# Kernel tuning notes

Measured on AMD Instinct MI355X. Metric: run time of the kernel, lower is better.

The kernel has to match this reference:

```python
import jax, jax.numpy as jnp
import numpy as np

B, C, N, IC = 4, 64, 4096, 32  # batch, in_channels(=g_channels), nodes, inter_channels


def setup_inputs() -> dict:
    key = jax.random.key(0)
    ks = jax.random.split(key, 8)
    s_c = (2.0 / C) ** 0.5   # kaiming-ish scales
    s_i = (2.0 / C) ** 0.5
    x = jax.random.normal(ks[0], (B, C, N), dtype=jnp.float32)
    g_w = jax.random.normal(ks[1], (C, C), dtype=jnp.float32) * s_c      # g: 1x1 conv (out=C, in=C)
    g_b = jnp.zeros((C,), dtype=jnp.float32)
    theta_w = jax.random.normal(ks[2], (IC, C), dtype=jnp.float32) * s_i  # theta: (out=IC, in=C)
    theta_b = jnp.zeros((IC,), dtype=jnp.float32)
    phi_w = jax.random.normal(ks[3], (IC, C), dtype=jnp.float32) * s_i
    phi_b = jnp.zeros((IC,), dtype=jnp.float32)
    cp_w = jax.random.normal(ks[4], (2 * IC,), dtype=jnp.float32) * (2.0 / (2 * IC)) ** 0.5  # concat_project 1x1 conv, no bias
    C_k = jnp.zeros((N, N), dtype=jnp.float32)  # learned adjacency bias, init zeros
    return {"x": x, "g_w": g_w, "g_b": g_b, "theta_w": theta_w, "theta_b": theta_b,
            "phi_w": phi_w, "phi_b": phi_b, "cp_w": cp_w, "C_k": C_k}


def reference(x, g_w, g_b, theta_w, theta_b, phi_w, phi_b, cp_w, C_k):
    # 1x1 convs are plain GEMMs over the node dim
    g_x = jnp.einsum('oc,bcn->bno', g_w, x) + g_b            # (B, N, C)
    th = jnp.einsum('oc,bcn->bon', theta_w, x) + theta_b[:, None]  # (B, IC, N)
    ph = jnp.einsum('oc,bcn->bon', phi_w, x) + phi_b[:, None]      # (B, IC, N)
    # concat_project on [theta_i ; phi_j] with a 1x1 conv is algebraically an outer sum:
    # f[b,i,j] = w_th . theta[b,:,i] + w_ph . phi[b,:,j]
    a = jnp.einsum('c,bcn->bn', cp_w[:IC], th)  # (B, N)
    p = jnp.einsum('c,bcn->bn', cp_w[IC:], ph)  # (B, N)
    f = a[:, :, None] + p[:, None, :]           # (B, N, N)
    attention = jax.nn.softmax(jax.nn.leaky_relu(f, negative_slope=0.2), axis=-1) + C_k
    y = jnp.einsum('bij,bjo->boi', attention, g_x)  # (B, C, N)
    return y
```

## Files before the change

kernel.cpp:

```cpp
#include <hip/hip_runtime.h>


#define B  4
#define C  64
#define N  4096
#define IC 32
#define NS 4104
#define NR 4097
#define MAGIC 0x13572468

#define OFF_FLAG   248
#define OFF_A      256
#define OFF_P      (OFF_A + B*N)
#define OFF_Q      (OFF_P + B*N)
#define OFF_PERM   (OFF_Q + B*N)
#define OFF_PRES   (OFF_PERM + B*N)
#define OFF_SUFS   (OFF_PRES + B*NS)
#define OFF_S1     (OFF_SUFS + B*NS)
#define OFF_S2     (OFF_S1 + B*64*64)
#define OFF_GX     (OFF_S2 + B*64*64)
#define OFF_PREG   (OFF_GX + B*N*64)
#define OFF_SUFG   (OFF_PREG + B*NR*64)

__global__ __launch_bounds__(256) void k1_gx(
    const float* __restrict__ x, const float* __restrict__ g_w,
    const float* __restrict__ g_b, const float* __restrict__ theta_w,
    const float* __restrict__ theta_b, const float* __restrict__ phi_w,
    const float* __restrict__ phi_b, const float* __restrict__ cp_w,
    const float* __restrict__ Ck, float* __restrict__ ws) {
  __shared__ float gwT[C * C];
  __shared__ float xl[C * 16];
  __shared__ float lu[C], lv[C], cst[2];
  const int tid = threadIdx.x;
  const int b = blockIdx.x >> 8;
  const int n0 = (blockIdx.x & 255) << 4;
  for (int idx = tid; idx < C * C; idx += 256) {
    int o = idx >> 6, cc = idx & 63;
    gwT[cc * C + o] = g_w[idx];
  }
  for (int idx = tid; idx < C * 16; idx += 256) {
    int cc = idx >> 4, nn = idx & 15;
    xl[idx] = x[(size_t)((b << 6) + cc) * N + n0 + nn];
  }
  if (tid < 64) {
    float u = 0.f;
    for (int k = 0; k < IC; ++k) u += cp_w[k] * theta_w[k * C + tid];
    lu[tid] = u;
  } else if (tid < 128) {
    int c = tid - 64;
    float v = 0.f;
    for (int k = 0; k < IC; ++k) v += cp_w[IC + k] * phi_w[k * C + c];
    lv[c] = v;
  } else if (tid == 128) {
    float ca = 0.f, cp2 = 0.f;
    for (int k = 0; k < IC; ++k) { ca += cp_w[k] * theta_b[k]; cp2 += cp_w[IC + k] * phi_b[k]; }
    cst[0] = ca; cst[1] = cp2;
  }
  __syncthreads();
  if (tid < 16) {
    float au = cst[0], pu = cst[1];
    for (int cc = 0; cc < C; ++cc) {
      float xv = xl[cc * 16 + tid];
      au += lu[cc] * xv;
      pu += lv[cc] * xv;
    }
    ws[OFF_A + (b << 12) + n0 + tid] = au;
    ws[OFF_P + (b << 12) + n0 + tid] = pu;
  }
  const int o = tid & 63, g4 = tid >> 6;
  float bb = g_b[o];
  float acc0 = bb, acc1 = bb, acc2 = bb, acc3 = bb;
  for (int cc = 0; cc < C; ++cc) {
    float gv = gwT[cc * C + o];
    const float* xr = &xl[cc * 16 + (g4 << 2)];
    acc0 += gv * xr[0]; acc1 += gv * xr[1]; acc2 += gv * xr[2]; acc3 += gv * xr[3];
  }
  float* gx = ws + OFF_GX + (size_t)((b << 12) + n0 + (g4 << 2)) * C + o;
  gx[0] = acc0; gx[64] = acc1; gx[128] = acc2; gx[192] = acc3;
  const float4* c4 = (const float4*)Ck;
  bool nz = false;
  int idx = (blockIdx.x << 8) + tid;
  for (int t = 0; t < 16; ++t) {
    float4 v = c4[idx];
    nz |= (v.x != 0.f) | (v.y != 0.f) | (v.z != 0.f) | (v.w != 0.f);
    idx += 262144;
  }
  if (__any(nz) && (tid & 63) == 0)
    atomicExch((int*)ws + OFF_FLAG, MAGIC);
}

__global__ __launch_bounds__(1024) void k2_rank(float* __restrict__ ws) {
  __shared__ float lp[N];
  __shared__ int partials[32][33];
  const int tid = threadIdx.x;
  const int b = blockIdx.x >> 7;
  const int rg = blockIdx.x & 127;
  const float* p = ws + OFF_P + b * N;
  ((float4*)lp)[tid] = ((const float4*)p)[tid];
  const int row = tid & 31, chunk = tid >> 5;
  const int i = (rg << 5) + row;
  __syncthreads();
  const float my = lp[i];
  const int c0 = chunk << 7;
  const float4* lp4 = (const float4*)(lp + c0);
  int r0 = 0, r1 = 0, r2 = 0, r3 = 0;
  for (int j = 0; j < 32; ++j) {
    float4 v = lp4[j];
    int k = c0 + (j << 2);
    r0 += (v.x < my) || (v.x == my && (k + 0) < i);
    r1 += (v.y < my) || (v.y == my && (k + 1) < i);
    r2 += (v.z < my) || (v.z == my && (k + 2) < i);
    r3 += (v.w < my) || (v.w == my && (k + 3) < i);
  }
  partials[row][chunk] = (r0 + r1) + (r2 + r3);
  __syncthreads();
  if (tid < 32) {
    int rank = 0;
#pragma unroll
    for (int c = 0; c < 32; ++c) rank += partials[tid][c];
    const int ii = (rg << 5) + tid;
    ws[OFF_Q + (b << 12) + rank] = lp[ii];
    ((int*)ws)[OFF_PERM + (b << 12) + rank] = ii;
  }
}

__global__ __launch_bounds__(1024) void k3_scan_chunks(float* __restrict__ ws) {
  __shared__ float sA[1024], sB[1024];
  const int tid = threadIdx.x;
  const int bid = blockIdx.x;
  if (bid < B) {
    const int b = bid;
    float* wt2 = sA;
    float* wt1 = sA + 16;
    float* wo2 = sA + 32;
    float* wo1 = sA + 49;
    const float* q = ws + OFF_Q + b * N;
    const float4 qv4 = ((const float4*)q)[tid];
    float e1r[4], e2r[4];
    e2r[0] = expf(0.2f * qv4.x); e1r[0] = expf(qv4.x);
    e2r[1] = expf(0.2f * qv4.y); e1r[1] = expf(qv4.y);
    e2r[2] = expf(0.2f * qv4.z); e1r[2] = expf(qv4.z);
    e2r[3] = expf(0.2f * qv4.w); e1r[3] = expf(qv4.w);
    float s2 = e2r[0] + e2r[1] + e2r[2] + e2r[3];
    float s1 = e1r[0] + e1r[1] + e1r[2] + e1r[3];
    const int lane = tid & 63, wave = tid >> 6;
    float x2 = s2, x1 = s1;
    for (int off = 1; off < 64; off <<= 1) {
      float t2 = __shfl_up(x2, off, 64);
      float t1 = __shfl_up(x1, off, 64);
      if (lane >= off) { x2 += t2; x1 += t1; }
    }
    if (lane == 63) { wt2[wave] = x2; wt1[wave] = x1; }
    __syncthreads();
    if (wave == 0 && lane < 17) {
      float a2 = 0.f, a1 = 0.f;
      for (int w = 0; w < 16; ++w) {
        if (w < lane) { a2 += wt2[w]; a1 += wt1[w]; }
      }
      wo2[lane] = a2; wo1[lane] = a1;
    }
    __syncthreads();
    const float excl2 = wo2[wave] + (x2 - s2);
    const float incl1 = wo1[wave] + x1;
    const float tot1 = wo1[16];
    float* PreS = ws + OFF_PRES + b * NS;
    float* SufS = ws + OFF_SUFS + b * NS;
    const int base = tid << 2;
    float run = excl2;
#pragma unroll
    for (int j = 0; j < 4; ++j) { PreS[base + j] = run; run += e2r[j]; }
    if (tid == 1023) PreS[N] = run;
    run = tot1 - incl1;
#pragma unroll
    for (int j = 3; j >= 0; --j) { run += e1r[j]; SufS[base + j] = run; }
    if (tid == 1023) SufS[N] = 0.f;
  } else {
    const int b2 = bid - B;
    const int b = b2 >> 6, c = b2 & 63;
    const int o = tid & 63, kk = tid >> 6;
    const float* q = ws + OFF_Q + b * N;
    const int* perm = (const int*)ws + OFF_PERM + b * N;
    const float* gx = ws + OFF_GX + ((size_t)b << 18);
    float p1 = 0.f, p2 = 0.f;
    const int k0 = (c << 6) + (kk << 2);
    for (int r = 0; r < 4; ++r) {
      int k = k0 + r;
      float qv = q[k];
      float g = gx[((size_t)perm[k] << 6) + o];
      p1 += expf(qv) * g;
      p2 += expf(0.2f * qv) * g;
    }
    sA[(kk << 6) + o] = p2;
    sB[(kk << 6) + o] = p1;
    __syncthreads();
    if (tid < 64) {
      float t2 = 0.f, t1 = 0.f;
#pragma unroll
      for (int g = 0; g < 16; ++g) { t2 += sA[(g << 6) + o]; t1 += sB[(g << 6) + o]; }
      ws[OFF_S2 + (size_t)(((b << 6) + c) << 6) + o] = t2;
      ws[OFF_S1 + (size_t)(((b << 6) + c) << 6) + o] = t1;
    }
  }
}

__global__ __launch_bounds__(1024) void k4_prefix(float* __restrict__ ws) {
  __shared__ float sA[1024], sB[1024];
  const int tid = threadIdx.x;
  const int b = blockIdx.x >> 6, c = blockIdx.x & 63;
  const int o = tid & 63, kk = tid >> 6;
  float offp = 0.f, offs = 0.f;
  {
    const float* S1 = ws + OFF_S1 + ((size_t)b << 12);
    const float* S2 = ws + OFF_S2 + ((size_t)b << 12);
    for (int cc = 0; cc < 64; ++cc) {
      float v2 = S2[(cc << 6) + o];
      float v1 = S1[(cc << 6) + o];
      offp += (cc < c) ? v2 : 0.f;
      offs += (cc > c) ? v1 : 0.f;
    }
  }
  const float* q = ws + OFF_Q + b * N;
  const int* perm = (const int*)ws + OFF_PERM + b * N;
  const float* gx = ws + OFF_GX + ((size_t)b << 18);
  float* PreG = ws + OFF_PREG + (size_t)b * NR * 64;
  float* SufG = ws + OFF_SUFG + (size_t)b * NR * 64;
  const int k0 = (c << 6) + (kk << 2);
  float w1[4], w2[4];
  float p1 = 0.f, p2 = 0.f;
  for (int r = 0; r < 4; ++r) {
    float qq = q[k0 + r];
    float gg = gx[((size_t)perm[k0 + r] << 6) + o];
    w1[r] = expf(qq) * gg;
    w2[r] = expf(0.2f * qq) * gg;
    p1 += w1[r]; p2 += w2[r];
  }
  sA[(kk << 6) + o] = p2;
  sB[(kk << 6) + o] = p1;
  __syncthreads();
  for (int kp = 0; kp < kk; ++kp) offp += sA[(kp << 6) + o];
  for (int kp = kk + 1; kp < 16; ++kp) offs += sB[(kp << 6) + o];
  float run = offp;
#pragma unroll
  for (int r = 0; r < 4; ++r) { PreG[(size_t)(k0 + r) * 64 + o] = run; run += w2[r]; }
  if (c == 63 && kk == 15) PreG[(size_t)N * 64 + o] = run;
  run = offs;
#pragma unroll
  for (int r = 3; r >= 0; --r) { run += w1[r]; SufG[(size_t)(k0 + r) * 64 + o] = run; }
  if (c == 0 && kk == 0) SufG[(size_t)N * 64 + o] = 0.f;
}

__global__ __launch_bounds__(1024) void k5_out(const float* __restrict__ Ck,
                                               float* __restrict__ ws,
                                               float* __restrict__ y) {
  __shared__ float lq[N];
  const int tid = threadIdx.x;
  const int b = blockIdx.x >> 6, rg = blockIdx.x & 63;
  const float4* qs = (const float4*)(ws + OFF_Q + b * N);
  ((float4*)lq)[tid] = qs[tid];
  __syncthreads();
  const int io = tid & 63, og = tid >> 6;
  const int i = (rg << 6) + io;
  float ai = ws[OFF_A + (b << 12) + i];
  float thr = -ai;
  int lo = 0, hi = N;
  while (lo < hi) { int m = (lo + hi) >> 1; if (lq[m] <= thr) lo = m + 1; else hi = m; }
  const int k = lo;
  float e1 = expf(ai), e2 = expf(0.2f * ai);
  float den = e1 * ws[OFF_SUFS + b * NS + k] + e2 * ws[OFF_PRES + b * NS + k];
  float inv = 1.0f / den;
  float4 pv = ((const float4*)(ws + OFF_PREG + ((size_t)b * NR + k) * 64))[og];
  float4 sv = ((const float4*)(ws + OFF_SUFG + ((size_t)b * NR + k) * 64))[og];
  float* yb = y + ((size_t)((b << 6) + (og << 2))) * N + i;
  yb[0]             = (e1 * sv.x + e2 * pv.x) * inv;
  yb[(size_t)N]     = (e1 * sv.y + e2 * pv.y) * inv;
  yb[(size_t)2 * N] = (e1 * sv.z + e2 * pv.z) * inv;
  yb[(size_t)3 * N] = (e1 * sv.w + e2 * pv.w) * inv;
  if (((const volatile int*)ws)[OFF_FLAG] == MAGIC) {
    __syncthreads();
    const int it = rg;
    const int o = tid & 63, jj = tid >> 6;
    const float* gx = ws + OFF_GX + ((size_t)b << 18);
    float (*red)[64] = (float(*)[64])lq;
    for (int ii = 0; ii < 64; ++ii) {
      int irow = (it << 6) + ii;
      float acc = 0.f;
      for (int j = jj; j < N; j += 16)
        acc += Ck[(size_t)irow * N + j] * gx[((size_t)j << 6) + o];
      red[jj][o] = acc;
      __syncthreads();
      if (jj == 0) {
        float s = 0.f;
#pragma unroll
        for (int g = 0; g < 16; ++g) s += red[g][o];
        y[((size_t)((b << 6) + o)) * N + irow] += s;
      }
      __syncthreads();
    }
  }
}

extern "C" void kernel_launch(void* const* d_in, const int* in_sizes, int n_in,
                              void* d_out, int out_size, void* d_ws, size_t ws_size,
                              hipStream_t stream) {
  (void)in_sizes; (void)n_in; (void)out_size; (void)ws_size;
  const float* x       = (const float*)d_in[0];
  const float* g_w     = (const float*)d_in[1];
  const float* g_b     = (const float*)d_in[2];
  const float* theta_w = (const float*)d_in[3];
  const float* theta_b = (const float*)d_in[4];
  const float* phi_w   = (const float*)d_in[5];
  const float* phi_b   = (const float*)d_in[6];
  const float* cp_w    = (const float*)d_in[7];
  const float* Ck      = (const float*)d_in[8];
  float* ws = (float*)d_ws;
  float* y  = (float*)d_out;

  hipLaunchKernelGGL(k1_gx, dim3(1024), dim3(256), 0, stream,
                     x, g_w, g_b, theta_w, theta_b, phi_w, phi_b, cp_w, Ck, ws);
  hipLaunchKernelGGL(k2_rank, dim3(512), dim3(1024), 0, stream, ws);
  hipLaunchKernelGGL(k3_scan_chunks, dim3(B + B * 64), dim3(1024), 0, stream, ws);
  hipLaunchKernelGGL(k4_prefix, dim3(B * 64), dim3(1024), 0, stream, ws);
  hipLaunchKernelGGL(k5_out, dim3(B * 64), dim3(1024), 0, stream, Ck, ws, y);
}
```

Measured before the change: 150.5 us.

## Fuse chunk scan and prefix kernels into one with redundant per-block chunk sums

Merges the scan/chunk-sum kernel and the prefix kernel into a single launch of 128 blocks. Each block recomputes the exp tables into LDS, every chunk sum for its batch, and the scalar prefix/suffix sums, then writes PreG/SufG for two chunks. This removes one kernel launch and the global round trip through S1/S2. In exchange each block redundantly gathers the whole batch's gx rows, about 1 MB per block, and the grid shrinks to 128 blocks.

```diff
diff --git a/kernel.cpp b/kernel.cpp
--- a/kernel.cpp
+++ b/kernel.cpp
@@ -124,129 +124,124 @@
   }
 }
 
-__global__ __launch_bounds__(1024) void k3_scan_chunks(float* __restrict__ ws) {
-  __shared__ float sA[1024], sB[1024];
+__global__ __launch_bounds__(1024) void k34_prefix(float* __restrict__ ws) {
+  __shared__ float smem[16384];
+  float* le1 = smem;
+  float* le2 = smem + 4096;
+  float* S1L = smem + 8192;
+  float* S2L = smem + 12288;
+  float* cs1  = S1L;
+  float* cs2  = S1L + 64;
+  float* cum1 = S1L + 128;
+  float* cum2 = S1L + 192;
+  float* tots = S1L + 256;
   const int tid = threadIdx.x;
-  const int bid = blockIdx.x;
-  if (bid < B) {
-    const int b = bid;
-    float* wt2 = sA;
-    float* wt1 = sA + 16;
-    float* wo2 = sA + 32;
-    float* wo1 = sA + 49;
-    const float* q = ws + OFF_Q + b * N;
-    const float4 qv4 = ((const float4*)q)[tid];
-    float e1r[4], e2r[4];
-    e2r[0] = expf(0.2f * qv4.x); e1r[0] = expf(qv4.x);
-    e2r[1] = expf(0.2f * qv4.y); e1r[1] = expf(qv4.y);
-    e2r[2] = expf(0.2f * qv4.z); e1r[2] = expf(qv4.z);
-    e2r[3] = expf(0.2f * qv4.w); e1r[3] = expf(qv4.w);
-    float s2 = e2r[0] + e2r[1] + e2r[2] + e2r[3];
-    float s1 = e1r[0] + e1r[1] + e1r[2] + e1r[3];
-    const int lane = tid & 63, wave = tid >> 6;
-    float x2 = s2, x1 = s1;
+  const int b = blockIdx.x >> 5, cg = blockIdx.x & 31;
+  const float* q = ws + OFF_Q + (b << 12);
+  const float4 q4 = ((const float4*)q)[tid];
+  const float e1r0 = expf(q4.x), e1r1 = expf(q4.y), e1r2 = expf(q4.z), e1r3 = expf(q4.w);
+  const float e2r0 = expf(0.2f * q4.x), e2r1 = expf(0.2f * q4.y),
+              e2r2 = expf(0.2f * q4.z), e2r3 = expf(0.2f * q4.w);
+  const int k4 = tid << 2;
+  float4 t1v = {e1r0, e1r1, e1r2, e1r3};
+  float4 t2v = {e2r0, e2r1, e2r2, e2r3};
+  *(float4*)&le1[k4] = t1v;
+  *(float4*)&le2[k4] = t2v;
+  float s1 = (e1r0 + e1r1) + (e1r2 + e1r3);
+  float s2 = (e2r0 + e2r1) + (e2r2 + e2r3);
+  for (int off = 8; off; off >>= 1) {
+    s1 += __shfl_down(s1, off, 16);
+    s2 += __shfl_down(s2, off, 16);
+  }
+  if ((tid & 15) == 0) { cs1[tid >> 4] = s1; cs2[tid >> 4] = s2; }
+  __syncthreads();
+  if (tid < 64) {
+    float a1s = 0.f, a2s = 0.f;
+    for (int c2 = 0; c2 < 64; ++c2) {
+      float v1 = cs1[c2], v2 = cs2[c2];
+      a1s += (c2 < tid) ? v1 : 0.f;
+      a2s += (c2 < tid) ? v2 : 0.f;
+    }
+    cum1[tid] = a1s; cum2[tid] = a2s;
+    if (tid == 63) { tots[0] = a1s + cs1[63]; tots[1] = a2s + cs2[63]; }
+  }
+  __syncthreads();
+  if (tid < 128) {
+    const int k = (cg << 7) + tid, c = k >> 6, lane = tid & 63;
+    float x1 = le1[k], x2 = le2[k];
+    const float e1v = x1, e2v = x2;
     for (int off = 1; off < 64; off <<= 1) {
-      float t2 = __shfl_up(x2, off, 64);
-      float t1 = __shfl_up(x1, off, 64);
-      if (lane >= off) { x2 += t2; x1 += t1; }
-    }
-    if (lane == 63) { wt2[wave] = x2; wt1[wave] = x1; }
-    __syncthreads();
-    if (wave == 0 && lane < 17) {
-      float a2 = 0.f, a1 = 0.f;
-      for (int w = 0; w < 16; ++w) {
-        if (w < lane) { a2 += wt2[w]; a1 += wt1[w]; }
-      }
-      wo2[lane] = a2; wo1[lane] = a1;
-    }
-    __syncthreads();
-    const float excl2 = wo2[wave] + (x2 - s2);
-    const float incl1 = wo1[wave] + x1;
-    const float tot1 = wo1[16];
-    float* PreS = ws + OFF_PRES + b * NS;
-    float* SufS = ws + OFF_SUFS + b * NS;
-    const int base = tid << 2;
-    float run = excl2;
-#pragma unroll
-    for (int j = 0; j < 4; ++j) { PreS[base + j] = run; run += e2r[j]; }
-    if (tid == 1023) PreS[N] = run;
-    run = tot1 - incl1;
-#pragma unroll
-    for (int j = 3; j >= 0; --j) { run += e1r[j]; SufS[base + j] = run; }
-    if (tid == 1023) SufS[N] = 0.f;
-  } else {
-    const int b2 = bid - B;
-    const int b = b2 >> 6, c = b2 & 63;
-    const int o = tid & 63, kk = tid >> 6;
-    const float* q = ws + OFF_Q + b * N;
-    const int* perm = (const int*)ws + OFF_PERM + b * N;
-    const float* gx = ws + OFF_GX + ((size_t)b << 18);
+      float u1 = __shfl_up(x1, off, 64);
+      float u2 = __shfl_up(x2, off, 64);
+      if (lane >= off) { x1 += u1; x2 += u2; }
+    }
+    ws[OFF_PRES + b * NS + k] = cum2[c] + (x2 - e2v);
+    ws[OFF_SUFS + b * NS + k] = tots[0] - (cum1[c] + (x1 - e1v));
+    if (cg == 31 && tid == 127) ws[OFF_PRES + b * NS + N] = tots[1];
+    if (cg == 0 && tid == 0)    ws[OFF_SUFS + b * NS + N] = 0.f;
+  }
+  __syncthreads();
+  const int l16 = tid & 15, krow = tid >> 4;
+  const int* perm = (const int*)ws + OFF_PERM + (b << 12);
+  const float* gx = ws + OFF_GX + ((size_t)b << 18);
+  float4 a1 = {0.f, 0.f, 0.f, 0.f}, a2 = {0.f, 0.f, 0.f, 0.f};
+  const int kb = krow << 6;
+  const int jrot = (krow & 3) << 4;
+  for (int jj = 0; jj < 64; ++jj) {
+    const int k = kb + ((jj + jrot) & 63);
+    const float4 g = *(const float4*)(gx + ((size_t)perm[k] << 6) + (l16 << 2));
+    const float e1 = le1[k], e2 = le2[k];
+    a1.x += e1 * g.x; a1.y += e1 * g.y; a1.z += e1 * g.z; a1.w += e1 * g.w;
+    a2.x += e2 * g.x; a2.y += e2 * g.y; a2.z += e2 * g.z; a2.w += e2 * g.w;
+  }
+  *(float4*)&S1L[(krow << 6) + (l16 << 2)] = a1;
+  *(float4*)&S2L[(krow << 6) + (l16 << 2)] = a2;
+  __syncthreads();
+  const int o = tid & 63, kk = tid >> 6;
+  const int c0 = cg << 1;
+  float op0 = 0.f, os0 = 0.f, op1 = 0.f, os1 = 0.f;
+  for (int cc = 0; cc < 64; ++cc) {
+    const float v2 = S2L[(cc << 6) + o];
+    const float v1 = S1L[(cc << 6) + o];
+    op0 += (cc < c0) ? v2 : 0.f;       os0 += (cc > c0) ? v1 : 0.f;
+    op1 += (cc <= c0) ? v2 : 0.f;      os1 += (cc > c0 + 1) ? v1 : 0.f;
+  }
+  __syncthreads();
+  float* sA = S1L;
+  float* sB = S1L + 1024;
+  float* PreG = ws + OFF_PREG + (size_t)b * NR * 64;
+  float* SufG = ws + OFF_SUFG + (size_t)b * NR * 64;
+#pragma unroll
+  for (int ci = 0; ci < 2; ++ci) {
+    const int c = c0 + ci;
+    const int k0 = (c << 6) + (kk << 2);
+    float w1[4], w2[4];
     float p1 = 0.f, p2 = 0.f;
-    const int k0 = (c << 6) + (kk << 2);
+#pragma unroll
     for (int r = 0; r < 4; ++r) {
-      int k = k0 + r;
-      float qv = q[k];
-      float g = gx[((size_t)perm[k] << 6) + o];
-      p1 += expf(qv) * g;
-      p2 += expf(0.2f * qv) * g;
+      const int k = k0 + r;
+      const float g = gx[((size_t)perm[k] << 6) + o];
+      w1[r] = le1[k] * g;
+      w2[r] = le2[k] * g;
+      p1 += w1[r]; p2 += w2[r];
     }
     sA[(kk << 6) + o] = p2;
     sB[(kk << 6) + o] = p1;
     __syncthreads();
-    if (tid < 64) {
-      float t2 = 0.f, t1 = 0.f;
-#pragma unroll
-      for (int g = 0; g < 16; ++g) { t2 += sA[(g << 6) + o]; t1 += sB[(g << 6) + o]; }
-      ws[OFF_S2 + (size_t)(((b << 6) + c) << 6) + o] = t2;
-      ws[OFF_S1 + (size_t)(((b << 6) + c) << 6) + o] = t1;
-    }
-  }
-}
-
-__global__ __launch_bounds__(1024) void k4_prefix(float* __restrict__ ws) {
-  __shared__ float sA[1024], sB[1024];
-  const int tid = threadIdx.x;
-  const int b = blockIdx.x >> 6, c = blockIdx.x & 63;
-  const int o = tid & 63, kk = tid >> 6;
-  float offp = 0.f, offs = 0.f;
-  {
-    const float* S1 = ws + OFF_S1 + ((size_t)b << 12);
-    const float* S2 = ws + OFF_S2 + ((size_t)b << 12);
-    for (int cc = 0; cc < 64; ++cc) {
-      float v2 = S2[(cc << 6) + o];
-      float v1 = S1[(cc << 6) + o];
-      offp += (cc < c) ? v2 : 0.f;
-      offs += (cc > c) ? v1 : 0.f;
-    }
-  }
-  const float* q = ws + OFF_Q + b * N;
-  const int* perm = (const int*)ws + OFF_PERM + b * N;
-  const float* gx = ws + OFF_GX + ((size_t)b << 18);
-  float* PreG = ws + OFF_PREG + (size_t)b * NR * 64;
-  float* SufG = ws + OFF_SUFG + (size_t)b * NR * 64;
-  const int k0 = (c << 6) + (kk << 2);
-  float w1[4], w2[4];
-  float p1 = 0.f, p2 = 0.f;
-  for (int r = 0; r < 4; ++r) {
-    float qq = q[k0 + r];
-    float gg = gx[((size_t)perm[k0 + r] << 6) + o];
-    w1[r] = expf(qq) * gg;
-    w2[r] = expf(0.2f * qq) * gg;
-    p1 += w1[r]; p2 += w2[r];
-  }
-  sA[(kk << 6) + o] = p2;
-  sB[(kk << 6) + o] = p1;
-  __syncthreads();
-  for (int kp = 0; kp < kk; ++kp) offp += sA[(kp << 6) + o];
-  for (int kp = kk + 1; kp < 16; ++kp) offs += sB[(kp << 6) + o];
-  float run = offp;
-#pragma unroll
-  for (int r = 0; r < 4; ++r) { PreG[(size_t)(k0 + r) * 64 + o] = run; run += w2[r]; }
-  if (c == 63 && kk == 15) PreG[(size_t)N * 64 + o] = run;
-  run = offs;
-#pragma unroll
-  for (int r = 3; r >= 0; --r) { run += w1[r]; SufG[(size_t)(k0 + r) * 64 + o] = run; }
-  if (c == 0 && kk == 0) SufG[(size_t)N * 64 + o] = 0.f;
+    float op = ci ? op1 : op0;
+    float os = ci ? os1 : os0;
+    for (int kp = 0; kp < kk; ++kp) op += sA[(kp << 6) + o];
+    for (int kp = kk + 1; kp < 16; ++kp) os += sB[(kp << 6) + o];
+    float run = op;
+#pragma unroll
+    for (int r = 0; r < 4; ++r) { PreG[(size_t)(k0 + r) * 64 + o] = run; run += w2[r]; }
+    if (c == 63 && kk == 15) PreG[(size_t)N * 64 + o] = run;
+    run = os;
+#pragma unroll
+    for (int r = 3; r >= 0; --r) { run += w1[r]; SufG[(size_t)(k0 + r) * 64 + o] = run; }
+    if (c == 0 && kk == 0) SufG[(size_t)N * 64 + o] = 0.f;
+    __syncthreads();
+  }
 }
 
 __global__ __launch_bounds__(1024) void k5_out(const float* __restrict__ Ck,
@@ -318,7 +313,6 @@
   hipLaunchKernelGGL(k1_gx, dim3(1024), dim3(256), 0, stream,
                      x, g_w, g_b, theta_w, theta_b, phi_w, phi_b, cp_w, Ck, ws);
   hipLaunchKernelGGL(k2_rank, dim3(512), dim3(1024), 0, stream, ws);
-  hipLaunchKernelGGL(k3_scan_chunks, dim3(B + B * 64), dim3(1024), 0, stream, ws);
-  hipLaunchKernelGGL(k4_prefix, dim3(B * 64), dim3(1024), 0, stream, ws);
+  hipLaunchKernelGGL(k34_prefix, dim3(B * 32), dim3(1024), 0, stream, ws);
   hipLaunchKernelGGL(k5_out, dim3(B * 64), dim3(1024), 0, stream, Ck, ws, y);
 }
```

Result: slower. 161.8 us (+7.5%).

## Spread the C_k nonzero scan across the first four kernels

Applied to the files above, without the earlier changes.

The full scan of the 64MB C_k matrix for nonzero entries used to sit in k1 as 16 sequential float4 loads per thread. It is now split into quarters, with k1, k2, k3 and k4 each loading one quarter early and checking it at the end. The aim is to overlap this bandwidth-bound read with each kernel's own compute and to issue the loads up front. The cost is more live registers and extra loads in the 1024-thread kernels.

```diff
diff --git a/kernel.cpp b/kernel.cpp
--- a/kernel.cpp
+++ b/kernel.cpp
@@ -8,6 +8,7 @@
 #define NS 4104
 #define NR 4097
 #define MAGIC 0x13572468
+#define CKQ 1048576
 
 #define OFF_FLAG   248
 #define OFF_A      256
@@ -22,6 +23,8 @@
 #define OFF_PREG   (OFF_GX + B*N*64)
 #define OFF_SUFG   (OFF_PREG + B*NR*64)
 
+#define CK_NZ(v) ((v.x != 0.f) | (v.y != 0.f) | (v.z != 0.f) | (v.w != 0.f))
+
 __global__ __launch_bounds__(256) void k1_gx(
     const float* __restrict__ x, const float* __restrict__ g_w,
     const float* __restrict__ g_b, const float* __restrict__ theta_w,
@@ -34,6 +37,13 @@
   const int tid = threadIdx.x;
   const int b = blockIdx.x >> 8;
   const int n0 = (blockIdx.x & 255) << 4;
+  const float4* c4 = (const float4*)Ck;
+  float4 ck0, ck1, ck2, ck3;
+  {
+    int idx = (blockIdx.x << 8) + tid;
+    ck0 = c4[idx]; ck1 = c4[idx + 262144];
+    ck2 = c4[idx + 524288]; ck3 = c4[idx + 786432];
+  }
   for (int idx = tid; idx < C * C; idx += 256) {
     int o = idx >> 6, cc = idx & 63;
     gwT[cc * C + o] = g_w[idx];
@@ -77,24 +87,24 @@
   }
   float* gx = ws + OFF_GX + (size_t)((b << 12) + n0 + (g4 << 2)) * C + o;
   gx[0] = acc0; gx[64] = acc1; gx[128] = acc2; gx[192] = acc3;
-  const float4* c4 = (const float4*)Ck;
-  bool nz = false;
-  int idx = (blockIdx.x << 8) + tid;
-  for (int t = 0; t < 16; ++t) {
-    float4 v = c4[idx];
-    nz |= (v.x != 0.f) | (v.y != 0.f) | (v.z != 0.f) | (v.w != 0.f);
-    idx += 262144;
-  }
+  bool nz = CK_NZ(ck0) | CK_NZ(ck1) | CK_NZ(ck2) | CK_NZ(ck3);
   if (__any(nz) && (tid & 63) == 0)
     atomicExch((int*)ws + OFF_FLAG, MAGIC);
 }
 
-__global__ __launch_bounds__(1024) void k2_rank(float* __restrict__ ws) {
+__global__ __launch_bounds__(1024) void k2_rank(const float* __restrict__ Ck,
+                                                float* __restrict__ ws) {
   __shared__ float lp[N];
   __shared__ int partials[32][33];
   const int tid = threadIdx.x;
   const int b = blockIdx.x >> 7;
   const int rg = blockIdx.x & 127;
+  const float4* c4 = (const float4*)Ck + CKQ;
+  float4 ck0, ck1;
+  {
+    int idx = (blockIdx.x << 10) + tid;
+    ck0 = c4[idx]; ck1 = c4[idx + 524288];
+  }
   const float* p = ws + OFF_P + b * N;
   ((float4*)lp)[tid] = ((const float4*)p)[tid];
   const int row = tid & 31, chunk = tid >> 5;
@@ -122,12 +132,25 @@
     ws[OFF_Q + (b << 12) + rank] = lp[ii];
     ((int*)ws)[OFF_PERM + (b << 12) + rank] = ii;
   }
-}
-
-__global__ __launch_bounds__(1024) void k3_scan_chunks(float* __restrict__ ws) {
+  bool nz = CK_NZ(ck0) | CK_NZ(ck1);
+  if (__any(nz) && (tid & 63) == 0)
+    atomicExch((int*)ws + OFF_FLAG, MAGIC);
+}
+
+__global__ __launch_bounds__(1024) void k3_scan_chunks(const float* __restrict__ Ck,
+                                                       float* __restrict__ ws) {
   __shared__ float sA[1024], sB[1024];
   const int tid = threadIdx.x;
   const int bid = blockIdx.x;
+  const float4* c4 = (const float4*)Ck + 2 * CKQ;
+  float4 ck0 = {0.f,0.f,0.f,0.f}, ck1 = ck0, ck2 = ck0, ck3 = ck0;
+  {
+    int idx = (bid << 10) + tid;
+    if (idx < CKQ) ck0 = c4[idx];  idx += 266240;
+    if (idx < CKQ) ck1 = c4[idx];  idx += 266240;
+    if (idx < CKQ) ck2 = c4[idx];  idx += 266240;
+    if (idx < CKQ) ck3 = c4[idx];
+  }
   if (bid < B) {
     const int b = bid;
     float* wt2 = sA;
@@ -201,13 +224,24 @@
       ws[OFF_S1 + (size_t)(((b << 6) + c) << 6) + o] = t1;
     }
   }
-}
-
-__global__ __launch_bounds__(1024) void k4_prefix(float* __restrict__ ws) {
+  bool nz = CK_NZ(ck0) | CK_NZ(ck1) | CK_NZ(ck2) | CK_NZ(ck3);
+  if (__any(nz) && (tid & 63) == 0)
+    atomicExch((int*)ws + OFF_FLAG, MAGIC);
+}
+
+__global__ __launch_bounds__(1024) void k4_prefix(const float* __restrict__ Ck,
+                                                  float* __restrict__ ws) {
   __shared__ float sA[1024], sB[1024];
   const int tid = threadIdx.x;
   const int b = blockIdx.x >> 6, c = blockIdx.x & 63;
   const int o = tid & 63, kk = tid >> 6;
+  const float4* c4 = (const float4*)Ck + 3 * CKQ;
+  float4 ck0, ck1, ck2, ck3;
+  {
+    int idx = (blockIdx.x << 10) + tid;
+    ck0 = c4[idx]; ck1 = c4[idx + 262144];
+    ck2 = c4[idx + 524288]; ck3 = c4[idx + 786432];
+  }
   float offp = 0.f, offs = 0.f;
   {
     const float* S1 = ws + OFF_S1 + ((size_t)b << 12);
@@ -247,6 +281,9 @@
 #pragma unroll
   for (int r = 3; r >= 0; --r) { run += w1[r]; SufG[(size_t)(k0 + r) * 64 + o] = run; }
   if (c == 0 && kk == 0) SufG[(size_t)N * 64 + o] = 0.f;
+  bool nz = CK_NZ(ck0) | CK_NZ(ck1) | CK_NZ(ck2) | CK_NZ(ck3);
+  if (__any(nz) && (tid & 63) == 0)
+    atomicExch((int*)ws + OFF_FLAG, MAGIC);
 }
 
 __global__ __launch_bounds__(1024) void k5_out(const float* __restrict__ Ck,
@@ -317,8 +354,8 @@
 
   hipLaunchKernelGGL(k1_gx, dim3(1024), dim3(256), 0, stream,
                      x, g_w, g_b, theta_w, theta_b, phi_w, phi_b, cp_w, Ck, ws);
-  hipLaunchKernelGGL(k2_rank, dim3(512), dim3(1024), 0, stream, ws);
-  hipLaunchKernelGGL(k3_scan_chunks, dim3(B + B * 64), dim3(1024), 0, stream, ws);
-  hipLaunchKernelGGL(k4_prefix, dim3(B * 64), dim3(1024), 0, stream, ws);
+  hipLaunchKernelGGL(k2_rank, dim3(512), dim3(1024), 0, stream, Ck, ws);
+  hipLaunchKernelGGL(k3_scan_chunks, dim3(B + B * 64), dim3(1024), 0, stream, Ck, ws);
+  hipLaunchKernelGGL(k4_prefix, dim3(B * 64), dim3(1024), 0, stream, Ck, ws);
   hipLaunchKernelGGL(k5_out, dim3(B * 64), dim3(1024), 0, stream, Ck, ws, y);
 }
```

Measured after the change: 150.2 us. About the same (-0.2%).
